# Kernel optimization log

Measured on AMD Instinct MI355X. Metric: run time of the kernel, lower is better.

## Reference

```python
import jax, jax.numpy as jnp
import numpy as np

N = 400000      # total atoms across batch of molecules
E = 1600000     # directed edges (avg degree 4)
G = 4096        # number of graphs (molecules)
F_IN = 78       # atomic feature size
H = 128         # gnn hidden dims (gnn_0 = gnn_1 = 128)
FF0, FF1 = 256, 128


def _lin(k, fan_in, fan_out):
    return jax.random.normal(k, (fan_in, fan_out), jnp.float32) / np.sqrt(fan_in).astype(np.float32)


def setup_inputs() -> dict:
    key = jax.random.key(0)
    ks = jax.random.split(key, 10)
    x = jax.random.normal(ks[0], (N, F_IN), jnp.float32)
    edge_index = jax.random.randint(ks[1], (2, E), 0, N, dtype=jnp.int64)
    # sorted graph ids, guaranteed non-empty segments (empty segment -> -inf under max pool)
    batch = (jnp.arange(N, dtype=jnp.int64) * G) // N
    return {
        'x': x, 'edge_index': edge_index, 'batch': batch,
        'W0': _lin(ks[2], F_IN, H), 'b0': jnp.zeros((H,), jnp.float32),
        'W1': _lin(ks[3], H, H),    'b1': jnp.zeros((H,), jnp.float32),
        'Wf0': _lin(ks[4], H, FF0), 'bf0': jnp.zeros((FF0,), jnp.float32),
        'Wf1': _lin(ks[5], FF0, FF1), 'bf1': jnp.zeros((FF1,), jnp.float32),
    }


def _gcn_conv(h, W, b, src, dst, dinv):
    # GCNConv with add_self_loops=True, symmetric normalization.
    hw = h @ W                                     # [N, out]
    norm = dinv[src] * dinv[dst]                   # [E]
    msg = hw[src] * norm[:, None]                  # gather + scale
    agg = jax.ops.segment_sum(msg, dst, num_segments=h.shape[0])
    agg = agg + hw * (dinv * dinv)[:, None]        # self-loop contribution
    return agg + b


def reference(x, edge_index, batch, W0, b0, W1, b1, Wf0, bf0, Wf1, bf1):
    src, dst = edge_index[0], edge_index[1]
    # degree of A + I computed at target nodes (PyG gcn_norm uses col)
    deg = jax.ops.segment_sum(jnp.ones((E,), x.dtype), dst, num_segments=N) + 1.0
    dinv = jax.lax.rsqrt(deg)

    h = jax.nn.relu(_gcn_conv(x, W0, b0, src, dst, dinv))
    h = jax.nn.relu(_gcn_conv(h, W1, b1, src, dst, dinv))

    g = jax.ops.segment_max(h, batch, num_segments=G)   # global max pool [G, H]

    g = jax.nn.relu(g @ Wf0 + bf0)   # dropout is identity in eval
    g = jax.nn.relu(g @ Wf1 + bf1)
    return g
```

## Files before the change

kernel.cpp:

```cpp
#include <hip/hip_runtime.h>
#include <cstdint>
#include <cstddef>

#define NATOMS 400000
#define NEDGES 1600000
#define NGRAPH 4096
#define F_INN  78
#define HDIM   128
#define FF0D   256
#define FF1D   128

typedef __attribute__((ext_vector_type(8))) short short8;
typedef __attribute__((ext_vector_type(4))) float f32x4;
typedef __attribute__((ext_vector_type(2))) float f32x2;

static __device__ __forceinline__ short f2bf(float f) {
    unsigned u = __builtin_bit_cast(unsigned, f);
    unsigned r = (u + 0x7fffu + ((u >> 16) & 1u)) >> 16;
    return (short)r;
}
static __device__ __forceinline__ float bf2f(unsigned short u) {
    return __builtin_bit_cast(float, ((unsigned)u) << 16);
}

__global__ __launch_bounds__(256) void k_degi(const int* __restrict__ dst,
                                              int* __restrict__ deg, int E) {
    int e = blockIdx.x * 256 + threadIdx.x;
    if (e < E) atomicAdd(&deg[dst[e]], 1);
}

__global__ __launch_bounds__(256) void k_dinv(const int* __restrict__ deg,
                                              float* __restrict__ dinv, int n) {
    int i = blockIdx.x * 256 + threadIdx.x;
    if (i < n) dinv[i] = rsqrtf((float)deg[i] + 1.0f);
}

__global__ __launch_bounds__(256) void k_scan1(int* __restrict__ data,
                                               int* __restrict__ blockSums, int n) {
    __shared__ int ts[256];
    const int base = blockIdx.x * 1024 + threadIdx.x * 4;
    int v[4];
    #pragma unroll
    for (int j = 0; j < 4; ++j) v[j] = (base + j < n) ? data[base + j] : 0;
    const int tot = v[0] + v[1] + v[2] + v[3];
    ts[threadIdx.x] = tot;
    __syncthreads();
    #pragma unroll
    for (int off = 1; off < 256; off <<= 1) {
        int t = (threadIdx.x >= off) ? ts[threadIdx.x - off] : 0;
        __syncthreads();
        ts[threadIdx.x] += t;
        __syncthreads();
    }
    int run = ts[threadIdx.x] - tot;
    #pragma unroll
    for (int j = 0; j < 4; ++j) {
        if (base + j < n) data[base + j] = run;
        run += v[j];
    }
    if (threadIdx.x == 255) blockSums[blockIdx.x] = ts[255];
}

__global__ __launch_bounds__(512) void k_scan2(int* __restrict__ blockSums, int nb) {
    __shared__ int ts[512];
    int v = (threadIdx.x < nb) ? blockSums[threadIdx.x] : 0;
    ts[threadIdx.x] = v;
    __syncthreads();
    #pragma unroll
    for (int off = 1; off < 512; off <<= 1) {
        int t = (threadIdx.x >= off) ? ts[threadIdx.x - off] : 0;
        __syncthreads();
        ts[threadIdx.x] += t;
        __syncthreads();
    }
    if (threadIdx.x < nb) blockSums[threadIdx.x] = ts[threadIdx.x] - v;
}

__global__ __launch_bounds__(256) void k_scan3(int* __restrict__ data,
                                               const int* __restrict__ blockSums,
                                               int* __restrict__ cursor,
                                               int n, int total) {
    const int off = blockSums[blockIdx.x];
    const int base = blockIdx.x * 1024 + threadIdx.x * 4;
    #pragma unroll
    for (int j = 0; j < 4; ++j)
        if (base + j < n) {
            int v = data[base + j] + off;
            data[base + j] = v;
            cursor[base + j] = v;
        }
    if (blockIdx.x == 0 && threadIdx.x == 0) data[n] = total;
}

__global__ __launch_bounds__(256) void k_fill(const int* __restrict__ src,
                                              const int* __restrict__ dst,
                                              int* __restrict__ cursor,
                                              int2* __restrict__ csr_ev,
                                              const float* __restrict__ dinv, int E) {
    int e = blockIdx.x * 256 + threadIdx.x;
    if (e >= E) return;
    int d = dst[e];
    int s = src[e];
    int pos = atomicAdd(&cursor[d], 1);
    float norm = dinv[s] * dinv[d];
    csr_ev[pos] = make_int2(s, __builtin_bit_cast(int, norm));
}

template<int KC, int KSRC>
__global__ __launch_bounds__(64) void k_packw(const float* __restrict__ W,
                                              short* __restrict__ wf) {
    int t = blockIdx.x * 64 + threadIdx.x;
    int f = t >> 6, lane = t & 63;
    int ct = f / KC, kc = f % KC;
    int n  = ct * 16 + (lane & 15);
    int k0 = kc * 32 + (lane >> 4) * 8;
    short8 o;
    #pragma unroll
    for (int j = 0; j < 8; ++j) {
        int k = k0 + j;
        float v = (k < KSRC) ? W[(size_t)k * 128 + n] : 0.f;
        o[j] = f2bf(v);
    }
    *(short8*)(wf + (size_t)t * 8) = o;
}

template<int KC, bool F32IN, int KSRC>
__global__ __launch_bounds__(256) void k_gemm_mfma(
    const void* __restrict__ inv, const short* __restrict__ wfrag,
    short* __restrict__ outp, int M)
{
    constexpr int RT = 5;
    const int wid  = threadIdx.x >> 6;
    const int lane = threadIdx.x & 63;
    const int m = lane & 15, q = lane >> 4;
    const int rowbase = blockIdx.x * (4 * RT * 16) + wid * (RT * 16);

    short8 bfr[8 * KC];
    #pragma unroll
    for (int f = 0; f < 8 * KC; ++f)
        bfr[f] = *(const short8*)(wfrag + ((size_t)(f * 64 + lane)) * 8);

    for (int rt = 0; rt < RT; ++rt) {
        const int rowa = rowbase + rt * 16 + m;
        short8 afr[KC];
        if constexpr (F32IN) {
            const float* xr = (const float*)inv + (size_t)rowa * KSRC;
            #pragma unroll
            for (int kc = 0; kc < KC; ++kc) {
                const int k0 = kc * 32 + q * 8;
                float v[8];
                #pragma unroll
                for (int j = 0; j < 8; ++j) v[j] = 0.f;
                if (k0 < KSRC) {
                    #pragma unroll
                    for (int p = 0; p < 4; ++p) {
                        int k = k0 + 2 * p;
                        if (k < KSRC) {
                            f32x2 t = __builtin_nontemporal_load((const f32x2*)(xr + k));
                            v[2 * p] = t.x; v[2 * p + 1] = t.y;
                        }
                    }
                }
                short8 a;
                #pragma unroll
                for (int j = 0; j < 8; ++j) a[j] = f2bf(v[j]);
                afr[kc] = a;
            }
        } else {
            const short* xr = (const short*)inv + (size_t)rowa * KSRC;
            #pragma unroll
            for (int kc = 0; kc < KC; ++kc)
                afr[kc] = __builtin_nontemporal_load((const short8*)(xr + kc * 32 + q * 8));
        }

        f32x4 acc[8];
        #pragma unroll
        for (int ct = 0; ct < 8; ++ct) acc[ct] = (f32x4){0.f, 0.f, 0.f, 0.f};
        #pragma unroll
        for (int kc = 0; kc < KC; ++kc)
            #pragma unroll
            for (int ct = 0; ct < 8; ++ct)
                acc[ct] = __builtin_amdgcn_mfma_f32_16x16x32_bf16(
                    afr[kc], bfr[ct * KC + kc], acc[ct], 0, 0, 0);

        #pragma unroll
        for (int ct = 0; ct < 8; ++ct)
            #pragma unroll
            for (int r = 0; r < 4; ++r) {
                int gr = rowbase + rt * 16 + q * 4 + r;
                outp[(size_t)gr * 128 + ct * 16 + m] = f2bf(acc[ct][r]);
            }
    }
}

__global__ __launch_bounds__(256) void k_gather_bf(
    const unsigned short* __restrict__ hw, unsigned short* __restrict__ agg,
    const int* __restrict__ row_start, const int2* __restrict__ csr_ev,
    const float* __restrict__ dinv, const float* __restrict__ bias, int Nn)
{
    const int n  = blockIdx.x * 16 + (threadIdx.x >> 4);
    const int c8 = (threadIdx.x & 15) * 8;
    const float dv = dinv[n];
    const float d2 = dv * dv;

    float acc[8];
    {
        const short8 sv = *(const short8*)(hw + (size_t)n * HDIM + c8);
        #pragma unroll
        for (int j = 0; j < 8; ++j)
            acc[j] = fmaf(bf2f((unsigned short)sv[j]), d2, bias[c8 + j]);
    }

    const int s0 = row_start[n], s1 = row_start[n + 1];
    int i = s0;
    for (; i + 1 < s1; i += 2) {
        const int2 e0 = csr_ev[i];
        const int2 e1 = csr_ev[i + 1];
        const short8 r0 = *(const short8*)(hw + (size_t)e0.x * HDIM + c8);
        const short8 r1 = *(const short8*)(hw + (size_t)e1.x * HDIM + c8);
        const float w0 = __builtin_bit_cast(float, e0.y);
        const float w1 = __builtin_bit_cast(float, e1.y);
        #pragma unroll
        for (int j = 0; j < 8; ++j) acc[j] = fmaf(bf2f((unsigned short)r0[j]), w0, acc[j]);
        #pragma unroll
        for (int j = 0; j < 8; ++j) acc[j] = fmaf(bf2f((unsigned short)r1[j]), w1, acc[j]);
    }
    if (i < s1) {
        const int2 e0 = csr_ev[i];
        const short8 r0 = *(const short8*)(hw + (size_t)e0.x * HDIM + c8);
        const float w0 = __builtin_bit_cast(float, e0.y);
        #pragma unroll
        for (int j = 0; j < 8; ++j) acc[j] = fmaf(bf2f((unsigned short)r0[j]), w0, acc[j]);
    }

    short8 o;
    #pragma unroll
    for (int j = 0; j < 8; ++j) o[j] = f2bf(fmaxf(acc[j], 0.f));
    __builtin_nontemporal_store(o, (short8*)(agg + (size_t)n * HDIM + c8));
}

__global__ __launch_bounds__(256) void k_pool(
    const unsigned short* __restrict__ agg,
    const int* __restrict__ batch, float* __restrict__ out, int Nn)
{
    __shared__ int se[2];
    __shared__ float red[256];
    int g = blockIdx.x;
    if (threadIdx.x < 2) {
        int target = g + (int)threadIdx.x;
        int lo = 0, hi = Nn;
        while (lo < hi) {
            int mid = (lo + hi) >> 1;
            if (batch[mid] < target) lo = mid + 1; else hi = mid;
        }
        se[threadIdx.x] = lo;
    }
    __syncthreads();
    const int start = se[0], end = se[1];
    const int c = threadIdx.x & 127;
    const int half = threadIdx.x >> 7;
    float m = 0.f;
    for (int i = start + half; i < end; i += 2)
        m = fmaxf(m, bf2f(__builtin_nontemporal_load(agg + (size_t)i * HDIM + c)));
    red[threadIdx.x] = m;
    __syncthreads();
    if (half == 0)
        out[(size_t)g * HDIM + c] = fmaxf(red[threadIdx.x], red[threadIdx.x + 128]);
}

template<int K, int NC, bool OUT_RELU_BIAS>
__global__ __launch_bounds__(256) void k_gemm(
    const float* __restrict__ in, const float* __restrict__ W,
    const float* __restrict__ out_bias, float* __restrict__ out0, int M)
{
    constexpr int BK = 32;
    constexpr int TC = NC / 8;
    constexpr int TR = 256 / TC;
    constexpr int ROWS = TR * 8;
    constexpr int XST = ROWS + 4;

    __shared__ float xs[BK][XST];
    __shared__ float ws[BK][NC];

    const int tid = threadIdx.x;
    const int tc  = tid % TC;
    const int tr  = tid / TC;
    const int row0 = blockIdx.x * ROWS;

    float acc[8][8];
    #pragma unroll
    for (int i = 0; i < 8; ++i)
        #pragma unroll
        for (int j = 0; j < 8; ++j) acc[i][j] = 0.f;

    for (int k0 = 0; k0 < K; k0 += BK) {
        {
            constexpr int TASKS = BK * NC / 4;
            #pragma unroll
            for (int it = 0; it < TASKS / 256; ++it) {
                int t  = it * 256 + tid;
                int wk = t / (NC / 4);
                int wc = (t % (NC / 4)) * 4;
                *(float4*)(&ws[wk][wc]) = *(const float4*)(W + (size_t)(k0 + wk) * NC + wc);
            }
        }
        {
            constexpr int TASKS = ROWS * BK / 4;
            #pragma unroll
            for (int it = 0; it < TASKS / 256; ++it) {
                int t   = it * 256 + tid;
                int r   = t / (BK / 4);
                int kq  = (t % (BK / 4)) * 4;
                float4 x4 = *(const float4*)(in + (size_t)(row0 + r) * K + k0 + kq);
                xs[kq + 0][r] = x4.x; xs[kq + 1][r] = x4.y;
                xs[kq + 2][r] = x4.z; xs[kq + 3][r] = x4.w;
            }
        }
        __syncthreads();
        #pragma unroll 8
        for (int kk = 0; kk < BK; ++kk) {
            float a[8], b[8];
            #pragma unroll
            for (int i = 0; i < 8; ++i) a[i] = xs[kk][tr * 8 + i];
            #pragma unroll
            for (int j = 0; j < 8; ++j) b[j] = ws[kk][tc * 8 + j];
            #pragma unroll
            for (int i = 0; i < 8; ++i)
                #pragma unroll
                for (int j = 0; j < 8; ++j)
                    acc[i][j] = fmaf(a[i], b[j], acc[i][j]);
        }
        __syncthreads();
    }

    #pragma unroll
    for (int i = 0; i < 8; ++i) {
        const int row = row0 + tr * 8 + i;
        #pragma unroll
        for (int jq = 0; jq < 2; ++jq) {
            const int col = tc * 8 + jq * 4;
            float4 v;
            v.x = acc[i][jq * 4 + 0]; v.y = acc[i][jq * 4 + 1];
            v.z = acc[i][jq * 4 + 2]; v.w = acc[i][jq * 4 + 3];
            if constexpr (OUT_RELU_BIAS) {
                const float4 bb = *(const float4*)(out_bias + col);
                v.x = fmaxf(v.x + bb.x, 0.f); v.y = fmaxf(v.y + bb.y, 0.f);
                v.z = fmaxf(v.z + bb.z, 0.f); v.w = fmaxf(v.w + bb.w, 0.f);
            }
            *(float4*)(out0 + (size_t)row * NC + col) = v;
        }
    }
}

extern "C" void kernel_launch(void* const* d_in, const int* in_sizes, int n_in,
                              void* d_out, int out_size, void* d_ws, size_t ws_size,
                              hipStream_t stream) {
    const float* x    = (const float*)d_in[0];
    const int*   ei   = (const int*)d_in[1];
    const int*   batch= (const int*)d_in[2];
    const float* W0   = (const float*)d_in[3];
    const float* b0   = (const float*)d_in[4];
    const float* W1   = (const float*)d_in[5];
    const float* b1   = (const float*)d_in[6];
    const float* Wf0  = (const float*)d_in[7];
    const float* bf0  = (const float*)d_in[8];
    const float* Wf1  = (const float*)d_in[9];
    const float* bf1  = (const float*)d_in[10];
    float* out = (float*)d_out;

    const int* srcI = ei;
    const int* dstI = ei + NEDGES;

    constexpr int SCAN_NBLK = (NATOMS + 1023) / 1024;

    unsigned short* hwA  = (unsigned short*)d_ws;
    unsigned short* aggB = hwA + (size_t)NATOMS * HDIM;
    float* dinv      = (float*)(aggB + (size_t)NATOMS * HDIM);
    int*   row_start = (int*)(dinv + NATOMS);
    int2*  csr_ev    = (int2*)(row_start + (NATOMS + 1) + 1);
    int*   cursor    = (int*)(csr_ev + NEDGES);
    int*   blockSums = cursor + NATOMS;
    float* pool      = (float*)(blockSums + 512);
    float* ff0       = pool + (size_t)NGRAPH * HDIM;
    short* wf0       = (short*)(ff0 + (size_t)NGRAPH * FF0D);
    short* wf1       = wf0 + 8 * 3 * 64 * 8;

    hipMemsetAsync(row_start, 0, (size_t)(NATOMS + 1) * sizeof(int), stream);
    k_degi<<<(NEDGES + 255) / 256, 256, 0, stream>>>(dstI, row_start, NEDGES);
    k_dinv<<<(NATOMS + 255) / 256, 256, 0, stream>>>(row_start, dinv, NATOMS);
    k_scan1<<<SCAN_NBLK, 256, 0, stream>>>(row_start, blockSums, NATOMS);
    k_scan2<<<1, 512, 0, stream>>>(blockSums, SCAN_NBLK);
    k_scan3<<<SCAN_NBLK, 256, 0, stream>>>(row_start, blockSums, cursor, NATOMS, NEDGES);
    k_fill<<<(NEDGES + 255) / 256, 256, 0, stream>>>(srcI, dstI, cursor, csr_ev, dinv, NEDGES);

    k_packw<3, F_INN><<<8 * 3, 64, 0, stream>>>(W0, wf0);
    k_packw<4, HDIM><<<8 * 4, 64, 0, stream>>>(W1, wf1);

    k_gemm_mfma<3, true, F_INN><<<1250, 256, 0, stream>>>(x, wf0, (short*)hwA, NATOMS);
    k_gather_bf<<<NATOMS / 16, 256, 0, stream>>>(hwA, aggB, row_start, csr_ev,
                                                 dinv, b0, NATOMS);

    k_gemm_mfma<4, false, HDIM><<<1250, 256, 0, stream>>>(aggB, wf1, (short*)hwA, NATOMS);
    k_gather_bf<<<NATOMS / 16, 256, 0, stream>>>(hwA, aggB, row_start, csr_ev,
                                                 dinv, b1, NATOMS);

    k_pool<<<NGRAPH, 256, 0, stream>>>(aggB, batch, pool, NATOMS);

    k_gemm<HDIM, FF0D, true><<<NGRAPH / 64, 256, 0, stream>>>(pool, Wf0, bf0, ff0, NGRAPH);
    k_gemm<FF0D, FF1D, true><<<NGRAPH / 128, 256, 0, stream>>>(ff0, Wf1, bf1, out, NGRAPH);
}
```

Baseline: 779.5 us.

## Record per-edge rank in degree pass to drop fill-phase atomics; fuse dinv into scan

The degree-counting kernel now stores the return value of each atomicAdd as a per-edge rank. The CSR fill computes each slot as row_start plus rank instead of doing a second atomic on a cursor array, and the cursor copy in scan3 is removed. The separate dinv kernel is folded into scan1. The rank buffer aliases the aggB workspace region, which is unused until after the fill, and workspace offsets are now hardcoded. The cost is an extra 6.4 MB write and read of rank versus the removed contended atomics.

```diff
diff --git a/kernel.cpp b/kernel.cpp
--- a/kernel.cpp
+++ b/kernel.cpp
@@ -24,24 +24,23 @@
 }
 
 __global__ __launch_bounds__(256) void k_degi(const int* __restrict__ dst,
-                                              int* __restrict__ deg, int E) {
+                                              int* __restrict__ deg,
+                                              int* __restrict__ rank, int E) {
     int e = blockIdx.x * 256 + threadIdx.x;
-    if (e < E) atomicAdd(&deg[dst[e]], 1);
-}
-
-__global__ __launch_bounds__(256) void k_dinv(const int* __restrict__ deg,
-                                              float* __restrict__ dinv, int n) {
-    int i = blockIdx.x * 256 + threadIdx.x;
-    if (i < n) dinv[i] = rsqrtf((float)deg[i] + 1.0f);
+    if (e < E) rank[e] = atomicAdd(&deg[dst[e]], 1);
 }
 
 __global__ __launch_bounds__(256) void k_scan1(int* __restrict__ data,
-                                               int* __restrict__ blockSums, int n) {
+                                               int* __restrict__ blockSums,
+                                               float* __restrict__ dinv, int n) {
     __shared__ int ts[256];
     const int base = blockIdx.x * 1024 + threadIdx.x * 4;
     int v[4];
     #pragma unroll
     for (int j = 0; j < 4; ++j) v[j] = (base + j < n) ? data[base + j] : 0;
+    #pragma unroll
+    for (int j = 0; j < 4; ++j)
+        if (base + j < n) dinv[base + j] = rsqrtf((float)v[j] + 1.0f);
     const int tot = v[0] + v[1] + v[2] + v[3];
     ts[threadIdx.x] = tot;
     __syncthreads();
@@ -78,30 +77,26 @@
 
 __global__ __launch_bounds__(256) void k_scan3(int* __restrict__ data,
                                                const int* __restrict__ blockSums,
-                                               int* __restrict__ cursor,
                                                int n, int total) {
     const int off = blockSums[blockIdx.x];
     const int base = blockIdx.x * 1024 + threadIdx.x * 4;
     #pragma unroll
     for (int j = 0; j < 4; ++j)
-        if (base + j < n) {
-            int v = data[base + j] + off;
-            data[base + j] = v;
-            cursor[base + j] = v;
-        }
+        if (base + j < n) data[base + j] += off;
     if (blockIdx.x == 0 && threadIdx.x == 0) data[n] = total;
 }
 
 __global__ __launch_bounds__(256) void k_fill(const int* __restrict__ src,
                                               const int* __restrict__ dst,
-                                              int* __restrict__ cursor,
+                                              const int* __restrict__ row_start,
+                                              const int* __restrict__ rank,
                                               int2* __restrict__ csr_ev,
                                               const float* __restrict__ dinv, int E) {
     int e = blockIdx.x * 256 + threadIdx.x;
     if (e >= E) return;
     int d = dst[e];
     int s = src[e];
-    int pos = atomicAdd(&cursor[d], 1);
+    int pos = row_start[d] + rank[e];
     float norm = dinv[s] * dinv[d];
     csr_ev[pos] = make_int2(s, __builtin_bit_cast(int, norm));
 }
@@ -373,25 +368,26 @@
 
     constexpr int SCAN_NBLK = (NATOMS + 1023) / 1024;
 
-    unsigned short* hwA  = (unsigned short*)d_ws;
-    unsigned short* aggB = hwA + (size_t)NATOMS * HDIM;
-    float* dinv      = (float*)(aggB + (size_t)NATOMS * HDIM);
-    int*   row_start = (int*)(dinv + NATOMS);
-    int2*  csr_ev    = (int2*)(row_start + (NATOMS + 1) + 1);
-    int*   cursor    = (int*)(csr_ev + NEDGES);
-    int*   blockSums = cursor + NATOMS;
-    float* pool      = (float*)(blockSums + 512);
-    float* ff0       = pool + (size_t)NGRAPH * HDIM;
-    short* wf0       = (short*)(ff0 + (size_t)NGRAPH * FF0D);
-    short* wf1       = wf0 + 8 * 3 * 64 * 8;
+    char* base = (char*)d_ws;
+    unsigned short* hwA  = (unsigned short*)(base + 0);
+    unsigned short* aggB = (unsigned short*)(base + 102400000);
+    int*   rank      = (int*)(base + 102400000);
+    float* dinv      = (float*)(base + 204800000);
+    int*   row_start = (int*)(base + 206400000);
+    int2*  csr_ev    = (int2*)(base + 208000064);
+    int*   blockSums = (int*)(base + 220800064);
+    float* pool      = (float*)(base + 220802112);
+    float* ff0       = (float*)(base + 222899264);
+    short* wf0       = (short*)(base + 227093568);
+    short* wf1       = (short*)(base + 227118144);
 
     hipMemsetAsync(row_start, 0, (size_t)(NATOMS + 1) * sizeof(int), stream);
-    k_degi<<<(NEDGES + 255) / 256, 256, 0, stream>>>(dstI, row_start, NEDGES);
-    k_dinv<<<(NATOMS + 255) / 256, 256, 0, stream>>>(row_start, dinv, NATOMS);
-    k_scan1<<<SCAN_NBLK, 256, 0, stream>>>(row_start, blockSums, NATOMS);
+    k_degi<<<(NEDGES + 255) / 256, 256, 0, stream>>>(dstI, row_start, rank, NEDGES);
+    k_scan1<<<SCAN_NBLK, 256, 0, stream>>>(row_start, blockSums, dinv, NATOMS);
     k_scan2<<<1, 512, 0, stream>>>(blockSums, SCAN_NBLK);
-    k_scan3<<<SCAN_NBLK, 256, 0, stream>>>(row_start, blockSums, cursor, NATOMS, NEDGES);
-    k_fill<<<(NEDGES + 255) / 256, 256, 0, stream>>>(srcI, dstI, cursor, csr_ev, dinv, NEDGES);
+    k_scan3<<<SCAN_NBLK, 256, 0, stream>>>(row_start, blockSums, NATOMS, NEDGES);
+    k_fill<<<(NEDGES + 255) / 256, 256, 0, stream>>>(srcI, dstI, row_start, rank,
+                                                     csr_ev, dinv, NEDGES);
 
     k_packw<3, F_INN><<<8 * 3, 64, 0, stream>>>(W0, wf0);
     k_packw<4, HDIM><<<8 * 4, 64, 0, stream>>>(W1, wf1);
```

After: 753.3 us. -3.4%, faster.
